# Optimization experiments

Hardware: AMD Instinct MI355X
Metric: run time of the kernel (lower is better)

## Reference

```python
import jax, jax.numpy as jnp
import numpy as np

MARGIN = 0.0
GAP = 0.4
N, D, C = 8192, 128, 10


def setup_inputs() -> dict:
    key = jax.random.key(0)
    k1, k2, k3 = jax.random.split(key, 3)
    inputs = jax.random.normal(k1, (N, D), dtype=jnp.float32)
    pred = jax.random.normal(k2, (N, C), dtype=jnp.float32)
    targets = jax.random.randint(k3, (N,), 0, C, dtype=jnp.int64)
    return {"inputs": inputs, "pred": pred, "targets": targets}


def reference(inputs, pred, targets):
    n = inputs.shape[0]
    # pairwise euclidean distances: ||xi||^2 + ||xj||^2 - 2 xi.xj, clamped + sqrt
    sq = jnp.sum(inputs * inputs, axis=1)                      # [n]
    dist = sq[:, None] + sq[None, :] - 2.0 * (inputs @ inputs.T)
    dist = jnp.sqrt(jnp.clip(dist, 1e-12))                     # [n, n]
    same = targets[:, None] == targets[None, :]                # [n, n] bool

    # confusion detection (original runs under no_grad)
    p = jax.nn.softmax(jax.lax.stop_gradient(pred), axis=1)
    val, top2 = jax.lax.top_k(p, 2)                            # [n,2]
    confuse = (val[:, 0] - val[:, 1] <= GAP) | (top2[:, 0] != targets)  # [n]

    # hard mining per row: hardest positive (max over same-class), hardest negative (min over diff-class)
    dist_ap = jnp.max(jnp.where(same, dist, -jnp.inf), axis=1)  # [n]
    dist_an = jnp.min(jnp.where(same, jnp.inf, dist), axis=1)   # [n]

    # MarginRankingLoss(margin=MARGIN) with y=1: mean(relu(-(an - ap) + margin)) over confused rows
    per_row = jnp.maximum(dist_ap - dist_an + MARGIN, 0.0)
    cnt = jnp.sum(confuse.astype(jnp.float32))
    loss = jnp.sum(jnp.where(confuse, per_row, 0.0)) / jnp.maximum(cnt, 1.0)
    return jnp.where(cnt > 0, loss, 0.0)
```

## Files before the change

### kernel.cpp

```cpp
#include <hip/hip_runtime.h>

#define NROWS 8192
#define DIMX  128
#define KB    192
#define KSEG  12
#define PTB   24576
#define NKS   3
#define NCLS  10
#define GAPV  0.4f
#define DEBIAS 504.03125f
#define SCL   (-0.0078125f)
#define RGR   256
#define NRG   (NROWS / RGR)
#define CHUNK 512
#define NCHUNK (NROWS / CHUNK)
#define NT    (CHUNK / 16)

typedef __attribute__((ext_vector_type(4))) int i32x4;

__device__ __forceinline__ int q8(float v) {
  int q = (int)rintf(16.f * v);
  return q > 127 ? 127 : (q < -127 ? -127 : q);
}

__global__ __launch_bounds__(256) void prep_k(const float* __restrict__ x,
                                              const int* __restrict__ tgt,
                                              const float* __restrict__ pred,
                                              char* __restrict__ xa,
                                              char* __restrict__ xbm,
                                              float* __restrict__ sq,
                                              int* __restrict__ conf,
                                              int* __restrict__ emin,
                                              int* __restrict__ emax,
                                              unsigned* __restrict__ ctrs) {
  if (blockIdx.x == 0 && threadIdx.x < 35) ctrs[threadIdx.x] = 0u;
  if (threadIdx.x < 4) {
    const int r = blockIdx.x * 4 + threadIdx.x;
    emin[r] = 0x7FFFFFFF;
    emax[r] = (int)0x80000000;
  }

  const int wave = threadIdx.x >> 6;
  const int lane = threadIdx.x & 63;
  const int row  = blockIdx.x * 4 + wave;
  const float2 f2 = ((const float2*)(x + (size_t)row * DIMX))[lane];
  float s = f2.x * f2.x + f2.y * f2.y;
  #pragma unroll
  for (int m = 1; m < 64; m <<= 1) s += __shfl_xor(s, m, 64);

  char* basea = xa  + (size_t)(row >> 7) * PTB + (size_t)(row & 127) * 16;
  char* baseb = xbm + (size_t)(row >> 7) * PTB + (size_t)(row & 127) * 16;
  {
    const int q0 = q8(f2.x), q1 = q8(f2.y);
    const unsigned short u = (unsigned short)((q0 & 0xFF) | ((q1 & 0xFF) << 8));
    const size_t off = (size_t)(lane >> 3) * 2048 + (lane & 7) * 2;
    *(unsigned short*)(basea + off) = u;
    *(unsigned short*)(baseb + off) = u;
  }
  const int cls = tgt[row];
  if (lane < 32) {
    const int j = 2 * lane;
    unsigned short ua, ub;
    if (lane < 20) {
      const int c = j >> 2;
      const bool hit = (c == cls);
      ua = hit ? (unsigned short)0x7F7F : 0;
      ub = hit ? (unsigned short)0x8181 : 0;
    } else if (lane == 20) {
      const int K = min((int)rintf(128.f * s), 32385);
      const int t = min(K / 127, 254);
      const int b1 = t < 127 ? t : 127;
      const int b2 = t - b1;
      ua = (unsigned short)0x7F7F;
      ub = (unsigned short)(((-b1) & 0xFF) | (((-b2) & 0xFF) << 8));
    } else if (lane == 21) {
      const int K = min((int)rintf(128.f * s), 32385);
      const int t = min(K / 127, 254);
      const int r = min(K - 127 * t, 126);
      ua = (unsigned short)0x0001;
      ub = (unsigned short)((-r) & 0xFF);
    } else { ua = 0; ub = 0; }
    const size_t off = (size_t)(8 + (j >> 4)) * 2048 + (j & 15);
    *(unsigned short*)(basea + off) = ua;
    *(unsigned short*)(baseb + off) = ub;
  }

  if (lane == 0) {
    sq[row] = s;
    const float* pp = pred + (size_t)row * NCLS;
    float v[NCLS];
    #pragma unroll
    for (int c = 0; c < NCLS; ++c) v[c] = pp[c];
    float m1 = v[0]; int i1 = 0;
    #pragma unroll
    for (int c = 1; c < NCLS; ++c)
      if (v[c] > m1) { m1 = v[c]; i1 = c; }
    float m2 = -INFINITY, sum = 0.f;
    #pragma unroll
    for (int c = 0; c < NCLS; ++c) {
      sum += __expf(v[c] - m1);
      if (c != i1) m2 = fmaxf(m2, v[c]);
    }
    const float d01 = (1.f - __expf(m2 - m1)) / sum;
    conf[row] = (d01 <= GAPV) || (i1 != cls);
  }
}

__global__ __launch_bounds__(256)
__attribute__((amdgpu_waves_per_eu(2, 8)))
void gram_k(const char* __restrict__ xa,
            const char* __restrict__ xbm,
            const float* __restrict__ sq,
            const int* __restrict__ conf,
            int* __restrict__ emin,
            int* __restrict__ emax,
            unsigned* __restrict__ ctrs,
            float* __restrict__ out) {
  __shared__ unsigned rg_last;
  __shared__ float red[2][4];
  const int tid  = threadIdx.x;
  const int wave = tid >> 6;
  const int lane = tid & 63;
  const int quad = lane >> 4;
  const int m16  = lane & 15;
  const int bx = blockIdx.x, by = blockIdx.y;

  i32x4 A[4][NKS];
  #pragma unroll
  for (int rt = 0; rt < 4; ++rt) {
    const int rbase = wave * 64 + rt * 16;
    const char* pa = xa + (size_t)(bx * 2 + (rbase >> 7)) * PTB
                        + (size_t)((rbase & 127) + m16) * 16;
    #pragma unroll
    for (int ks = 0; ks < NKS; ++ks)
      A[rt][ks] = *(const i32x4*)(pa + (size_t)(ks * 4 + quad) * 2048);
  }
  #pragma unroll
  for (int rt = 0; rt < 4; ++rt)
    #pragma unroll
    for (int ks = 0; ks < NKS; ++ks)
      asm("" : "+v"(A[rt][ks]));

  int Emin[4][4], Emax[4][4];
  #pragma unroll
  for (int r = 0; r < 4; ++r)
    #pragma unroll
    for (int q = 0; q < 4; ++q) { Emin[r][q] = 0x7FFFFFFF; Emax[r][q] = (int)0x80000000; }

  const char* bl = xbm + (size_t)(by * 4) * PTB + (size_t)m16 * 16 + (size_t)quad * 2048;

  i32x4 Bc[NKS], Bn[NKS];
  #pragma unroll
  for (int ks = 0; ks < NKS; ++ks) Bc[ks] = *(const i32x4*)(bl + ks * 8192);

  for (int s = 0; s < NT / 4; ++s) {
    #pragma unroll
    for (int jt = 0; jt < 4; ++jt) {
      const int u  = s * 4 + jt;
      const int un = (u + 1 < NT) ? u + 1 : NT - 1;
      const size_t toff = (size_t)(un >> 3) * PTB + (size_t)(un & 7) * 256;
      #pragma unroll
      for (int ks = 0; ks < NKS; ++ks)
        Bn[ks] = *(const i32x4*)(bl + toff + ks * 8192);

      i32x4 acc[4];
      #pragma unroll
      for (int r = 0; r < 4; ++r) acc[r] = (i32x4){0, 0, 0, 0};
      #pragma unroll
      for (int ks = 0; ks < NKS; ++ks)
        #pragma unroll
        for (int r = 0; r < 4; ++r)
          acc[r] = __builtin_amdgcn_mfma_i32_16x16x64_i8(A[r][ks], Bc[ks], acc[r], 0, 0, 0);

      #pragma unroll
      for (int r = 0; r < 4; ++r)
        #pragma unroll
        for (int q = 0; q < 4; ++q) {
          Emin[r][q] = min(Emin[r][q], acc[r][q]);
          Emax[r][q] = max(Emax[r][q], acc[r][q]);
        }

      #pragma unroll
      for (int ks = 0; ks < NKS; ++ks) Bc[ks] = Bn[ks];
    }
  }

  #pragma unroll
  for (int m = 1; m <= 8; m <<= 1)
    #pragma unroll
    for (int r = 0; r < 4; ++r)
      #pragma unroll
      for (int q = 0; q < 4; ++q) {
        Emin[r][q] = min(Emin[r][q], __shfl_xor(Emin[r][q], m, 64));
        Emax[r][q] = max(Emax[r][q], __shfl_xor(Emax[r][q], m, 64));
      }

  if (m16 == 0) {
    const int rowb = bx * RGR + wave * 64 + quad * 4;
    #pragma unroll
    for (int r = 0; r < 4; ++r)
      #pragma unroll
      for (int q = 0; q < 4; ++q) {
        atomicMin(&emin[rowb + r * 16 + q], Emin[r][q]);
        atomicMax(&emax[rowb + r * 16 + q], Emax[r][q]);
      }
  }

  asm volatile("s_waitcnt vmcnt(0)" ::: "memory");
  __syncthreads();
  if (tid == 0)
    rg_last = (atomicAdd(&ctrs[3 + bx], 1u) == NCHUNK - 1u) ? 1u : 0u;
  __syncthreads();
  if (rg_last) {
    const int row = bx * RGR + tid;
    const int lo = atomicAdd(&emin[row], 0);
    const int hi = atomicAdd(&emax[row], 0);
    float ps = 0.f, pc = 0.f;
    if (conf[row]) {
      const float ap = sqrtf(fmaxf(sq[row] + SCL * (float)lo - DEBIAS, 1e-12f));
      const float an = sqrtf(fmaxf(sq[row] + SCL * (float)hi, 1e-12f));
      ps = fmaxf(ap - an, 0.f);
      pc = 1.f;
    }
    #pragma unroll
    for (int m = 1; m < 64; m <<= 1) {
      ps += __shfl_xor(ps, m, 64);
      pc += __shfl_xor(pc, m, 64);
    }
    if (lane == 0) { red[0][wave] = ps; red[1][wave] = pc; }
    __syncthreads();
    if (tid == 0) {
      float* Ssum = (float*)(ctrs + 1);
      float* Csum = (float*)(ctrs + 2);
      atomicAdd(Ssum, red[0][0] + red[0][1] + red[0][2] + red[0][3]);
      atomicAdd(Csum, red[1][0] + red[1][1] + red[1][2] + red[1][3]);
      asm volatile("s_waitcnt vmcnt(0)" ::: "memory");
      if (atomicAdd(&ctrs[0], 1u) == NRG - 1u) {
        const float St = atomicAdd(Ssum, 0.f);
        const float Ct = atomicAdd(Csum, 0.f);
        out[0] = (Ct > 0.f) ? (St / fmaxf(Ct, 1.f)) : 0.f;
      }
    }
  }
}

extern "C" void kernel_launch(void* const* d_in, const int* in_sizes, int n_in,
                              void* d_out, int out_size, void* d_ws, size_t ws_size,
                              hipStream_t stream) {
  const float* x    = (const float*)d_in[0];
  const float* pred = (const float*)d_in[1];
  const int*   tgt  = (const int*)d_in[2];
  float* out = (float*)d_out;

  char* w = (char*)d_ws;
  const size_t arr_bytes = (size_t)NROWS * KB;
  char*  xa   = w;
  char*  xbm  = w + arr_bytes;
  float* sq   = (float*)(w + 2 * arr_bytes);
  int*   conf = (int*)(w + 2 * arr_bytes + (size_t)NROWS * 4);
  int*   emin = (int*)(w + 2 * arr_bytes + (size_t)NROWS * 8);
  int*   emax = (int*)(w + 2 * arr_bytes + (size_t)NROWS * 12);
  unsigned* ctrs = (unsigned*)(w + 2 * arr_bytes + (size_t)NROWS * 16);

  hipLaunchKernelGGL(prep_k, dim3(NROWS / 4), dim3(256), 0, stream,
                     x, tgt, pred, xa, xbm, sq, conf, emin, emax, ctrs);
  hipLaunchKernelGGL(gram_k, dim3(NRG, NCHUNK), dim3(256), 0, stream,
                     xa, xbm, sq, conf, emin, emax, ctrs, out);
}
```

Baseline: 83.83 us.

## Restructure prep kernel to process 32 rows per block with LDS-staged 16-byte stores

Rewrites the preprocessing kernel so each 256-thread block handles 32 rows. Each thread loads float4 vectors, packs them to int8, and stages the results in shared memory so they can be written to the panel layout as coalesced 16-byte stores. The old version wrote scattered 2-byte stores. The class, norm and padding segments are now written as full 16-byte vectors per row by a single thread. The aim is fewer, wider global writes and fewer blocks. The cost is a shared-memory barrier and only 32 active threads for the tail work, including the softmax confusion step.

New measurement: 83.05 us, median of 2. Within noise of the previous version (-0.9%).

```diff
diff --git a/kernel.cpp b/kernel.cpp
--- a/kernel.cpp
+++ b/kernel.cpp
@@ -15,12 +15,17 @@
 #define CHUNK 512
 #define NCHUNK (NROWS / CHUNK)
 #define NT    (CHUNK / 16)
+#define PRW   32
 
 typedef __attribute__((ext_vector_type(4))) int i32x4;
 
 __device__ __forceinline__ int q8(float v) {
   int q = (int)rintf(16.f * v);
   return q > 127 ? 127 : (q < -127 ? -127 : q);
+}
+__device__ __forceinline__ int pk4(float4 v) {
+  return (q8(v.x) & 255) | ((q8(v.y) & 255) << 8) |
+         ((q8(v.z) & 255) << 16) | ((q8(v.w) & 255) << 24);
 }
 
 __global__ __launch_bounds__(256) void prep_k(const float* __restrict__ x,
@@ -33,60 +38,73 @@
                                               int* __restrict__ emin,
                                               int* __restrict__ emax,
                                               unsigned* __restrict__ ctrs) {
-  if (blockIdx.x == 0 && threadIdx.x < 35) ctrs[threadIdx.x] = 0u;
-  if (threadIdx.x < 4) {
-    const int r = blockIdx.x * 4 + threadIdx.x;
-    emin[r] = 0x7FFFFFFF;
-    emax[r] = (int)0x80000000;
-  }
-
-  const int wave = threadIdx.x >> 6;
-  const int lane = threadIdx.x & 63;
-  const int row  = blockIdx.x * 4 + wave;
-  const float2 f2 = ((const float2*)(x + (size_t)row * DIMX))[lane];
-  float s = f2.x * f2.x + f2.y * f2.y;
-  #pragma unroll
-  for (int m = 1; m < 64; m <<= 1) s += __shfl_xor(s, m, 64);
-
-  char* basea = xa  + (size_t)(row >> 7) * PTB + (size_t)(row & 127) * 16;
-  char* baseb = xbm + (size_t)(row >> 7) * PTB + (size_t)(row & 127) * 16;
+  __shared__ char  pan[8 * PRW * 16];
+  __shared__ float ssq[PRW];
+  const int tid = threadIdx.x;
+  const int blk = blockIdx.x;
+  if (blk == 0 && tid < 35) ctrs[tid] = 0u;
+
   {
-    const int q0 = q8(f2.x), q1 = q8(f2.y);
-    const unsigned short u = (unsigned short)((q0 & 0xFF) | ((q1 & 0xFF) << 8));
-    const size_t off = (size_t)(lane >> 3) * 2048 + (lane & 7) * 2;
-    *(unsigned short*)(basea + off) = u;
-    *(unsigned short*)(baseb + off) = u;
-  }
-  const int cls = tgt[row];
-  if (lane < 32) {
-    const int j = 2 * lane;
-    unsigned short ua, ub;
-    if (lane < 20) {
-      const int c = j >> 2;
-      const bool hit = (c == cls);
-      ua = hit ? (unsigned short)0x7F7F : 0;
-      ub = hit ? (unsigned short)0x8181 : 0;
-    } else if (lane == 20) {
-      const int K = min((int)rintf(128.f * s), 32385);
-      const int t = min(K / 127, 254);
-      const int b1 = t < 127 ? t : 127;
-      const int b2 = t - b1;
-      ua = (unsigned short)0x7F7F;
-      ub = (unsigned short)(((-b1) & 0xFF) | (((-b2) & 0xFF) << 8));
-    } else if (lane == 21) {
-      const int K = min((int)rintf(128.f * s), 32385);
-      const int t = min(K / 127, 254);
-      const int r = min(K - 127 * t, 126);
-      ua = (unsigned short)0x0001;
-      ub = (unsigned short)((-r) & 0xFF);
-    } else { ua = 0; ub = 0; }
-    const size_t off = (size_t)(8 + (j >> 4)) * 2048 + (j & 15);
-    *(unsigned short*)(basea + off) = ua;
-    *(unsigned short*)(baseb + off) = ub;
-  }
-
-  if (lane == 0) {
-    sq[row] = s;
+    const int r32 = tid >> 3;
+    const int sg  = tid & 7;
+    const float4* xr = (const float4*)(x + (size_t)(blk * PRW + r32) * DIMX) + sg * 4;
+    float ss = 0.f;
+    i32x4 w;
+    #pragma unroll
+    for (int k = 0; k < 4; ++k) {
+      const float4 v = xr[k];
+      ss += v.x * v.x + v.y * v.y + v.z * v.z + v.w * v.w;
+      w[k] = pk4(v);
+    }
+    *(i32x4*)&pan[(sg * PRW + r32) * 16] = w;
+    ss += __shfl_xor(ss, 1, 64);
+    ss += __shfl_xor(ss, 2, 64);
+    ss += __shfl_xor(ss, 4, 64);
+    if (sg == 0) ssq[r32] = ss;
+  }
+  __syncthreads();
+
+  const int panel = blk >> 2;
+  const int rbase = (blk & 3) * PRW;
+
+  {
+    const int kseg = tid >> 5;
+    const int r32  = tid & 31;
+    const i32x4 w = *(const i32x4*)&pan[(kseg * PRW + r32) * 16];
+    const size_t off = (size_t)panel * PTB + (size_t)kseg * 2048 + (size_t)(rbase + r32) * 16;
+    *(i32x4*)(xa + off)  = w;
+    *(i32x4*)(xbm + off) = w;
+  }
+
+  if (tid < PRW) {
+    const int row = blk * PRW + tid;
+    const float s = ssq[tid];
+    const int cls = tgt[row];
+    const int K  = min((int)rintf(128.f * s), 32385);
+    const int t2 = min(K / 127, 254);
+    const int b1 = t2 < 127 ? t2 : 127;
+    const int b2 = t2 - b1;
+    const int rr = min(K - 127 * t2, 126);
+
+    i32x4 a8 = {0,0,0,0}, a9 = {0,0,0,0}, a10 = {0,0,0,0}, z = {0,0,0,0};
+    i32x4 b8 = {0,0,0,0}, b9 = {0,0,0,0}, b10 = {0,0,0,0};
+    if (cls < 4)      { a8[cls]      = 0x7F7F7F7F; b8[cls]      = (int)0x81818181; }
+    else if (cls < 8) { a9[cls - 4]  = 0x7F7F7F7F; b9[cls - 4]  = (int)0x81818181; }
+    else              { a10[cls - 8] = 0x7F7F7F7F; b10[cls - 8] = (int)0x81818181; }
+    a10[2] = 0x00017F7F;
+    b10[2] = ((-b1) & 255) | (((-b2) & 255) << 8) | (((-rr) & 255) << 16);
+
+    char* pa = xa  + (size_t)panel * PTB + (size_t)(rbase + tid) * 16;
+    char* pb = xbm + (size_t)panel * PTB + (size_t)(rbase + tid) * 16;
+    *(i32x4*)(pa +  8 * 2048) = a8;  *(i32x4*)(pb +  8 * 2048) = b8;
+    *(i32x4*)(pa +  9 * 2048) = a9;  *(i32x4*)(pb +  9 * 2048) = b9;
+    *(i32x4*)(pa + 10 * 2048) = a10; *(i32x4*)(pb + 10 * 2048) = b10;
+    *(i32x4*)(pa + 11 * 2048) = z;   *(i32x4*)(pb + 11 * 2048) = z;
+
+    sq[row]   = s;
+    emin[row] = 0x7FFFFFFF;
+    emax[row] = (int)0x80000000;
+
     const float* pp = pred + (size_t)row * NCLS;
     float v[NCLS];
     #pragma unroll
@@ -262,7 +280,7 @@
   int*   emax = (int*)(w + 2 * arr_bytes + (size_t)NROWS * 12);
   unsigned* ctrs = (unsigned*)(w + 2 * arr_bytes + (size_t)NROWS * 16);
 
-  hipLaunchKernelGGL(prep_k, dim3(NROWS / 4), dim3(256), 0, stream,
+  hipLaunchKernelGGL(prep_k, dim3(NROWS / PRW), dim3(256), 0, stream,
                      x, tgt, pred, xa, xbm, sq, conf, emin, emax, ctrs);
   hipLaunchKernelGGL(gram_k, dim3(NRG, NCHUNK), dim3(256), 0, stream,
                      xa, xbm, sq, conf, emin, emax, ctrs, out);
```
